# Kernel optimization log

Measured on AMD Instinct MI355X. Metric: run time of the kernel, lower is better.

The kernel has to match this reference:

```python
import jax, jax.numpy as jnp
import numpy as np

N_HEADS = 16
D_MODEL = 1024
TOTAL = 8192
N_SEQ = 8
SEQ_LEN = TOTAL // N_SEQ


def setup_inputs() -> dict:
    key = jax.random.key(0)
    ks = jax.random.split(key, 12)
    f = jnp.float32
    d = D_MODEL
    inp = {
        "query": jax.random.normal(ks[0], (TOTAL, d), f),
        "key": jax.random.normal(ks[1], (TOTAL, d), f),
        "value": jax.random.normal(ks[2], (TOTAL, d), f),
        "seq_lengths_q": jnp.full((N_SEQ,), SEQ_LEN, jnp.int64 if jax.config.jax_enable_x64 else jnp.int32),
        "seq_lengths_kv": jnp.full((N_SEQ,), SEQ_LEN, jnp.int64 if jax.config.jax_enable_x64 else jnp.int32),
        "Wq": jax.random.normal(ks[3], (d, d), f) * 0.02,
        "bq": jnp.zeros((d,), f),
        "Wk": jax.random.normal(ks[4], (d, d), f) * 0.02,
        "bk": jnp.zeros((d,), f),
        "Wv": jax.random.normal(ks[5], (d, d), f) * 0.02,
        "bv": jnp.zeros((d,), f),
        "Wo": jax.random.normal(ks[6], (d, d), f) * 0.02,
        "bo": jnpp if False else jnp.zeros((d,), f),
    }
    return inp


def reference(query, key, value, seq_lengths_q, seq_lengths_kv, Wq, bq, Wk, bk, Wv, bv, Wo, bo):
    Tq, d = query.shape
    Tkv = key.shape[0]
    H = N_HEADS
    Dh = d // H
    B = seq_lengths_q.shape[0]
    Lq = Tq // B  # equal-length packed sequences
    Lkv = Tkv // B
    scale = 1.0 / jnp.sqrt(jnp.asarray(Dh, query.dtype))

    # torch Linear: x @ W.T + b
    Q = (query @ Wq.T + bq).reshape(H, Tq, Dh)   # NOTE: raw view, no transpose
    K = (key @ Wk.T + bk).reshape(H, Tkv, Dh)    # (replicates original's view semantics)
    V = (value @ Wv.T + bv).reshape(H, Tkv, Dh)

    # Block-diagonal mask over equal-length sequences == per-block attention.
    Qb = Q.reshape(H, B, Lq, Dh)
    Kb = K.reshape(H, B, Lkv, Dh)
    Vb = V.reshape(H, B, Lkv, Dh)

    scores = jnp.einsum("hbqd,hbkd->hbqk", Qb, Kb) * scale  # [H,B,Lq,Lkv]
    probs = jax.nn.softmax(scores, axis=-1)
    attn = jnp.einsum("hbqk,hbkd->hbqd", probs, Vb)          # [H,B,Lq,Dh]

    attn = attn.reshape(H, Tq, Dh).reshape(Tq, d)  # matches .view(total_q, d_model)
    out = attn @ Wo.T + bo
    return out
```

## Files before the change

### kernel.cpp

```cpp
#include <hip/hip_runtime.h>
#include <hip/hip_bf16.h>

#define TOTAL   8192
#define DMODEL  1024
#define NHEADS  16
#define NSEQ    8
#define DH      64

typedef float  f32x4 __attribute__((ext_vector_type(4)));
typedef short  s16x8 __attribute__((ext_vector_type(8)));
typedef unsigned short u16;
typedef u16    u16x8 __attribute__((ext_vector_type(8)));
typedef unsigned int u32;
typedef u32    u32x4 __attribute__((ext_vector_type(4)));

__device__ __forceinline__ u16 f2bf_rne(float x) {
  union { float f; unsigned u; } v; v.f = x;
  unsigned r = v.u + 0x7FFFu + ((v.u >> 16) & 1u);
  return (u16)(r >> 16);
}

__device__ __forceinline__ u32 pk_hu(float a, float b) {
  union { float f; u32 u; } A, B; A.f = a; B.f = b;
  return __builtin_amdgcn_perm(B.u + 0x8000u, A.u + 0x8000u, 0x07060302u);
}

__device__ __forceinline__ void async_cp16(const u16* g, u16* l) {
  __builtin_amdgcn_global_load_lds(
      (const __attribute__((address_space(1))) unsigned int*)g,
      (__attribute__((address_space(3))) unsigned int*)l, 16, 0, 0);
}

__device__ __forceinline__ void cvt8_one(const float* __restrict__ src,
                                         u16* __restrict__ dst, long i) {
  float4 a = *reinterpret_cast<const float4*>(src + i);
  float4 b = *reinterpret_cast<const float4*>(src + i + 4);
  u16x8 o;
  o[0] = f2bf_rne(a.x); o[1] = f2bf_rne(a.y); o[2] = f2bf_rne(a.z); o[3] = f2bf_rne(a.w);
  o[4] = f2bf_rne(b.x); o[5] = f2bf_rne(b.y); o[6] = f2bf_rne(b.z); o[7] = f2bf_rne(b.w);
  *reinterpret_cast<u16x8*>(dst + i) = o;
}

__global__ __launch_bounds__(256) void cvt8_w4(const float* __restrict__ w0,
                                               const float* __restrict__ w1,
                                               const float* __restrict__ w2,
                                               const float* __restrict__ w3,
                                               u16* __restrict__ dst) {
  const float* srcs[4] = {w0, w1, w2, w3};
  cvt8_one(srcs[blockIdx.y], dst + (long)blockIdx.y * (DMODEL * (long)DMODEL),
           ((long)blockIdx.x * 256 + threadIdx.x) * 8);
}

__global__ __launch_bounds__(256) void gemm_qkv_f32a(const float* __restrict__ Xq,
                                                     const float* __restrict__ Xk,
                                                     const float* __restrict__ Xv,
                                                     const u16*  __restrict__ W3,
                                                     const float* __restrict__ bq,
                                                     const float* __restrict__ bk,
                                                     const float* __restrict__ bv,
                                                     u16* __restrict__ QKV) {
  __shared__ u16 As[128 * 32];
  __shared__ u16 Bs[128 * 32];
  const int z = blockIdx.z;
  const float* X    = (z == 0) ? Xq : (z == 1) ? Xk : Xv;
  const float* bias = (z == 0) ? bq : (z == 1) ? bk : bv;
  const u16* B = W3 + (long)z * (DMODEL * (long)DMODEL);
  u16* C = QKV + (long)z * (TOTAL * (long)DMODEL);

  const int tid  = threadIdx.x;
  const int lane = tid & 63;
  const int wv   = tid >> 6;
  const int quad = lane >> 4;
  const int m16  = lane & 15;
  const int wm   = (wv & 1) * 64;
  const int wn   = (wv >> 1) * 64;
  const long bm0 = (long)blockIdx.x * 128;
  const long bn0 = (long)blockIdx.y * 128;

  const int arow = tid >> 1;
  const int acol = (tid & 1) * 16;
  const int srow = lane >> 2;
  const int sk8  = (lane & 3) * 8;

  f32x4 acc[4][4] = {};
  const float* Abase = X + (bm0 + arow) * (long)DMODEL + acol;
  const u16*   Bbase = B + bn0 * DMODEL;

  for (int k0 = 0; k0 < DMODEL; k0 += 32) {
    #pragma unroll
    for (int j = 0; j < 2; j++) {
      const int r = j * 4 + wv;
      async_cp16(Bbase + (long)(r * 16 + srow) * DMODEL + k0 + sk8, &Bs[r * 512]);
    }
    {
      const float4* ga = (const float4*)(Abase + k0);
      float4 x0 = ga[0], x1 = ga[1], x2 = ga[2], x3 = ga[3];
      u32x4 p0, p1;
      p0[0] = pk_hu(x0.x, x0.y); p0[1] = pk_hu(x0.z, x0.w);
      p0[2] = pk_hu(x1.x, x1.y); p0[3] = pk_hu(x1.z, x1.w);
      p1[0] = pk_hu(x2.x, x2.y); p1[1] = pk_hu(x2.z, x2.w);
      p1[2] = pk_hu(x3.x, x3.y); p1[3] = pk_hu(x3.z, x3.w);
      *(u32x4*)&As[arow * 32 + acol]     = p0;
      *(u32x4*)&As[arow * 32 + acol + 8] = p1;
    }
    __syncthreads();

    s16x8 af[4], bfr[4];
    #pragma unroll
    for (int i = 0; i < 4; i++)
      af[i] = *(const s16x8*)&As[(wm + i * 16 + m16) * 32 + quad * 8];
    #pragma unroll
    for (int j = 0; j < 4; j++)
      bfr[j] = *(const s16x8*)&Bs[(wn + j * 16 + m16) * 32 + quad * 8];
    #pragma unroll
    for (int i = 0; i < 4; i++)
      #pragma unroll
      for (int j = 0; j < 4; j++)
        acc[i][j] = __builtin_amdgcn_mfma_f32_16x16x32_bf16(af[i], bfr[j], acc[i][j], 0, 0, 0);
    __syncthreads();
  }

  #pragma unroll
  for (int j = 0; j < 4; j++) {
    const long col = bn0 + wn + j * 16 + m16;
    const float bj = bias[col];
    #pragma unroll
    for (int i = 0; i < 4; i++) {
      const long row0 = bm0 + wm + i * 16 + quad * 4;
      #pragma unroll
      for (int r = 0; r < 4; r++)
        C[(row0 + r) * DMODEL + col] = f2bf_rne(acc[i][j][r] + bj);
    }
  }
}

__global__ __launch_bounds__(256) void gemm_out64(const u16* __restrict__ A,
                                                  const u16* __restrict__ B,
                                                  const float* __restrict__ bias,
                                                  float* __restrict__ C) {
  __shared__ u16 As[128 * 64];
  __shared__ u16 Bs[128 * 64];
  const int tid  = threadIdx.x;
  const int lane = tid & 63;
  const int wv   = tid >> 6;
  const int quad = lane >> 4;
  const int m16  = lane & 15;
  const int wm   = (wv & 1) * 64;
  const int wn   = (wv >> 1) * 64;
  const long bm0 = (long)blockIdx.x * 128;
  const long bn0 = (long)blockIdx.y * 128;

  const int r8 = lane >> 3;
  const int c8 = (lane & 7) * 8;

  f32x4 acc[4][4] = {};
  const u16* Abase = A + bm0 * DMODEL;
  const u16* Bbase = B + bn0 * DMODEL;

  for (int k0 = 0; k0 < DMODEL; k0 += 64) {
    #pragma unroll
    for (int j = 0; j < 4; j++) {
      const int rr = j * 4 + wv;
      const long row = rr * 8 + r8;
      async_cp16(Abase + row * DMODEL + k0 + c8, &As[rr * 512]);
      async_cp16(Bbase + row * DMODEL + k0 + c8, &Bs[rr * 512]);
    }
    __syncthreads();

    #pragma unroll
    for (int ks = 0; ks < 2; ks++) {
      s16x8 af[4], bfr[4];
      #pragma unroll
      for (int i = 0; i < 4; i++)
        af[i] = *(const s16x8*)&As[(wm + i * 16 + m16) * 64 + ks * 32 + quad * 8];
      #pragma unroll
      for (int j = 0; j < 4; j++)
        bfr[j] = *(const s16x8*)&Bs[(wn + j * 16 + m16) * 64 + ks * 32 + quad * 8];
      #pragma unroll
      for (int i = 0; i < 4; i++)
        #pragma unroll
        for (int j = 0; j < 4; j++)
          acc[i][j] = __builtin_amdgcn_mfma_f32_16x16x32_bf16(af[i], bfr[j], acc[i][j], 0, 0, 0);
    }
    __syncthreads();
  }

  #pragma unroll
  for (int j = 0; j < 4; j++) {
    const long col = bn0 + wn + j * 16 + m16;
    const float bj = bias[col];
    #pragma unroll
    for (int i = 0; i < 4; i++) {
      const long row0 = bm0 + wm + i * 16 + quad * 4;
      #pragma unroll
      for (int r = 0; r < 4; r++)
        C[(row0 + r) * DMODEL + col] = acc[i][j][r] + bj;
    }
  }
}

__global__ __launch_bounds__(256) void transpose_v(const u16* __restrict__ Vbf,
                                                   u16* __restrict__ Vt) {
  constexpr int TP = 72;
  __shared__ u16 tile[64 * TP];
  const int tid = threadIdx.x;
  const long base = (long)blockIdx.y * 65536;
  const int kt = blockIdx.x;
  {
    int k = tid >> 2, dh0 = (tid & 3) * 16;
    const u16* g = Vbf + base + (long)(kt * 64 + k) * 64 + dh0;
    u16x8 a = ((const u16x8*)g)[0];
    u16x8 b = ((const u16x8*)g)[1];
    #pragma unroll
    for (int i = 0; i < 8; i++) tile[(dh0 + i) * TP + k] = a[i];
    #pragma unroll
    for (int i = 0; i < 8; i++) tile[(dh0 + 8 + i) * TP + k] = b[i];
  }
  __syncthreads();
  {
    int dh = tid >> 2, k0 = (tid & 3) * 16;
    u16x8 a = *(const u16x8*)&tile[dh * TP + k0];
    u16x8 b = *(const u16x8*)&tile[dh * TP + k0 + 8];
    u16* g = Vt + base + (long)dh * 1024 + kt * 64 + k0;
    ((u16x8*)g)[0] = a;
    ((u16x8*)g)[1] = b;
  }
}

__global__ __launch_bounds__(256) void attn_kernel(const u16* __restrict__ Qbf,
                                                   const u16* __restrict__ Kbf,
                                                   const u16* __restrict__ Vt,
                                                   u16* __restrict__ Obf) {
  constexpr int KP = 72;
  __shared__ u16 Ks[64 * KP];
  __shared__ u16 Vs[64 * KP];
  __shared__ u16 Es[4 * 32 * KP];
  const int tid  = threadIdx.x;
  const int lane = tid & 63;
  const int wv   = tid >> 6;
  const int quad = lane >> 4;
  const int m16  = lane & 15;
  const int qt   = blockIdx.y;
  const long base = (long)blockIdx.x * 65536;

  const int qrow0 = qt * 128 + wv * 32;
  s16x8 aq[2][2];
  #pragma unroll
  for (int g = 0; g < 2; g++)
    #pragma unroll
    for (int s = 0; s < 2; s++)
      aq[g][s] = *(const s16x8*)(Qbf + base + (long)(qrow0 + g * 16 + m16) * 64 + s * 32 + quad * 8);

  f32x4 acc_o[2][4] = {};
  f32x4 acc_d[2] = {};

  union { u16x8 u; s16x8 s; } onesu;
  u16 ov = (m16 == 0) ? (u16)0x3F80 : (u16)0;
  #pragma unroll
  for (int i = 0; i < 8; i++) onesu.u[i] = ov;
  const s16x8 bones = onesu.s;

  const float SC = 0.125f * 1.44269504088896340736f;
  const int sr = tid >> 2;
  const int sk = (tid & 3) * 16;

  for (int nt = 0; nt < 16; nt++) {
    {
      const u16* g = Kbf + base + nt * 4096 + (long)sr * 64 + sk;
      u16x8 a = ((const u16x8*)g)[0];
      u16x8 b = ((const u16x8*)g)[1];
      *(u16x8*)&Ks[sr * KP + sk]     = a;
      *(u16x8*)&Ks[sr * KP + sk + 8] = b;
    }
    {
      const u16* g = Vt + base + (long)sr * 1024 + nt * 64 + sk;
      u16x8 a = ((const u16x8*)g)[0];
      u16x8 b = ((const u16x8*)g)[1];
      *(u16x8*)&Vs[sr * KP + sk]     = a;
      *(u16x8*)&Vs[sr * KP + sk + 8] = b;
    }
    __syncthreads();

    #pragma unroll
    for (int n = 0; n < 4; n++) {
      s16x8 bk0 = *(const s16x8*)&Ks[(n * 16 + m16) * KP + quad * 8];
      s16x8 bk1 = *(const s16x8*)&Ks[(n * 16 + m16) * KP + 32 + quad * 8];
      #pragma unroll
      for (int g = 0; g < 2; g++) {
        f32x4 s = {0.f, 0.f, 0.f, 0.f};
        s = __builtin_amdgcn_mfma_f32_16x16x32_bf16(aq[g][0], bk0, s, 0, 0, 0);
        s = __builtin_amdgcn_mfma_f32_16x16x32_bf16(aq[g][1], bk1, s, 0, 0, 0);
        #pragma unroll
        for (int r = 0; r < 4; r++) {
          float e = __builtin_amdgcn_exp2f(s[r] * SC);
          Es[(wv * 32 + g * 16 + quad * 4 + r) * KP + n * 16 + m16] = f2bf_rne(e);
        }
      }
    }
    s16x8 ae[2][2];
    #pragma unroll
    for (int g = 0; g < 2; g++) {
      ae[g][0] = *(const s16x8*)&Es[(wv * 32 + g * 16 + m16) * KP + quad * 8];
      ae[g][1] = *(const s16x8*)&Es[(wv * 32 + g * 16 + m16) * KP + 32 + quad * 8];
    }
    #pragma unroll
    for (int n = 0; n < 4; n++) {
      s16x8 bv0 = *(const s16x8*)&Vs[(n * 16 + m16) * KP + quad * 8];
      s16x8 bv1 = *(const s16x8*)&Vs[(n * 16 + m16) * KP + 32 + quad * 8];
      #pragma unroll
      for (int g = 0; g < 2; g++) {
        acc_o[g][n] = __builtin_amdgcn_mfma_f32_16x16x32_bf16(ae[g][0], bv0, acc_o[g][n], 0, 0, 0);
        acc_o[g][n] = __builtin_amdgcn_mfma_f32_16x16x32_bf16(ae[g][1], bv1, acc_o[g][n], 0, 0, 0);
      }
    }
    #pragma unroll
    for (int g = 0; g < 2; g++) {
      acc_d[g] = __builtin_amdgcn_mfma_f32_16x16x32_bf16(ae[g][0], bones, acc_d[g], 0, 0, 0);
      acc_d[g] = __builtin_amdgcn_mfma_f32_16x16x32_bf16(ae[g][1], bones, acc_d[g], 0, 0, 0);
    }
    __syncthreads();
  }

  #pragma unroll
  for (int g = 0; g < 2; g++)
    #pragma unroll
    for (int r = 0; r < 4; r++) {
      float d = __shfl(acc_d[g][r], lane & 48);
      float rinv = 1.0f / d;
      const long orow = base + (long)(qrow0 + g * 16 + quad * 4 + r) * 64;
      #pragma unroll
      for (int n = 0; n < 4; n++)
        Obf[orow + n * 16 + m16] = f2bf_rne(acc_o[g][n][r] * rinv);
    }
}

extern "C" void kernel_launch(void* const* d_in, const int* in_sizes, int n_in,
                              void* d_out, int out_size, void* d_ws, size_t ws_size,
                              hipStream_t stream) {
  const float* query = (const float*)d_in[0];
  const float* key_  = (const float*)d_in[1];
  const float* value = (const float*)d_in[2];
  const float* Wq = (const float*)d_in[5];
  const float* bq = (const float*)d_in[6];
  const float* Wk = (const float*)d_in[7];
  const float* bk = (const float*)d_in[8];
  const float* Wv = (const float*)d_in[9];
  const float* bv = (const float*)d_in[10];
  const float* Wo = (const float*)d_in[11];
  const float* bo = (const float*)d_in[12];

  char* ws = (char*)d_ws;
  u16* Wbf = (u16*)(ws);
  u16* QKV = (u16*)(ws + (8l << 20));
  u16* Qbf = QKV;
  u16* Kbf = QKV + 1 * (TOTAL * (long)DMODEL);
  u16* Vbf = QKV + 2 * (TOTAL * (long)DMODEL);
  u16* Vt  = (u16*)(ws + (56l << 20));
  u16* Obf = Vbf;

  cvt8_w4<<<dim3(512, 4), 256, 0, stream>>>(Wq, Wk, Wv, Wo, Wbf);
  gemm_qkv_f32a<<<dim3(64, 8, 3), 256, 0, stream>>>(query, key_, value, Wbf,
                                                    bq, bk, bv, QKV);
  transpose_v<<<dim3(16, 128), 256, 0, stream>>>(Vbf, Vt);
  attn_kernel<<<dim3(128, 8), 256, 0, stream>>>(Qbf, Kbf, Vt, Obf);
  gemm_out64<<<dim3(64, 8), 256, 0, stream>>>(Obf, Wbf + 3 * 1048576, bo, (float*)d_out);
}
```

Before: 349.8 us.

## Pre-convert QKV inputs to bf16 and shrink output GEMM tile to 64x128

Adds a separate kernel that converts query/key/value to bf16 before the QKV projection, so the GEMM can load A tiles with async global-to-LDS copies instead of loading fp32 and converting in registers. The output projection GEMM uses 64x128 tiles, doubling the number of blocks. This trades an extra full pass over the activations (read fp32, write bf16) for a simpler, async-loaded GEMM main loop and better occupancy in the output GEMM.

Result: no change. 345.6 us (-1.2%).

```diff
diff --git a/kernel.cpp b/kernel.cpp
--- a/kernel.cpp
+++ b/kernel.cpp
@@ -11,18 +11,11 @@
 typedef short  s16x8 __attribute__((ext_vector_type(8)));
 typedef unsigned short u16;
 typedef u16    u16x8 __attribute__((ext_vector_type(8)));
-typedef unsigned int u32;
-typedef u32    u32x4 __attribute__((ext_vector_type(4)));
 
 __device__ __forceinline__ u16 f2bf_rne(float x) {
   union { float f; unsigned u; } v; v.f = x;
   unsigned r = v.u + 0x7FFFu + ((v.u >> 16) & 1u);
   return (u16)(r >> 16);
-}
-
-__device__ __forceinline__ u32 pk_hu(float a, float b) {
-  union { float f; u32 u; } A, B; A.f = a; B.f = b;
-  return __builtin_amdgcn_perm(B.u + 0x8000u, A.u + 0x8000u, 0x07060302u);
 }
 
 __device__ __forceinline__ void async_cp16(const u16* g, u16* l) {
@@ -51,19 +44,26 @@
            ((long)blockIdx.x * 256 + threadIdx.x) * 8);
 }
 
-__global__ __launch_bounds__(256) void gemm_qkv_f32a(const float* __restrict__ Xq,
-                                                     const float* __restrict__ Xk,
-                                                     const float* __restrict__ Xv,
-                                                     const u16*  __restrict__ W3,
-                                                     const float* __restrict__ bq,
-                                                     const float* __restrict__ bk,
-                                                     const float* __restrict__ bv,
-                                                     u16* __restrict__ QKV) {
+__global__ __launch_bounds__(256) void cvt8_x3(const float* __restrict__ x0,
+                                               const float* __restrict__ x1,
+                                               const float* __restrict__ x2,
+                                               u16* __restrict__ dst) {
+  const float* srcs[3] = {x0, x1, x2};
+  cvt8_one(srcs[blockIdx.y], dst + (long)blockIdx.y * (TOTAL * (long)DMODEL),
+           ((long)blockIdx.x * 256 + threadIdx.x) * 8);
+}
+
+__global__ __launch_bounds__(256) void gemm_qkv(const u16* __restrict__ X3,
+                                                const u16* __restrict__ W3,
+                                                const float* __restrict__ bq,
+                                                const float* __restrict__ bk,
+                                                const float* __restrict__ bv,
+                                                u16* __restrict__ QKV) {
   __shared__ u16 As[128 * 32];
   __shared__ u16 Bs[128 * 32];
   const int z = blockIdx.z;
-  const float* X    = (z == 0) ? Xq : (z == 1) ? Xk : Xv;
   const float* bias = (z == 0) ? bq : (z == 1) ? bk : bv;
+  const u16* A = X3 + (long)z * (TOTAL * (long)DMODEL);
   const u16* B = W3 + (long)z * (DMODEL * (long)DMODEL);
   u16* C = QKV + (long)z * (TOTAL * (long)DMODEL);
 
@@ -77,31 +77,20 @@
   const long bm0 = (long)blockIdx.x * 128;
   const long bn0 = (long)blockIdx.y * 128;
 
-  const int arow = tid >> 1;
-  const int acol = (tid & 1) * 16;
   const int srow = lane >> 2;
   const int sk8  = (lane & 3) * 8;
 
   f32x4 acc[4][4] = {};
-  const float* Abase = X + (bm0 + arow) * (long)DMODEL + acol;
-  const u16*   Bbase = B + bn0 * DMODEL;
+  const u16* Abase = A + bm0 * DMODEL;
+  const u16* Bbase = B + bn0 * DMODEL;
 
   for (int k0 = 0; k0 < DMODEL; k0 += 32) {
     #pragma unroll
     for (int j = 0; j < 2; j++) {
-      const int r = j * 4 + wv;
-      async_cp16(Bbase + (long)(r * 16 + srow) * DMODEL + k0 + sk8, &Bs[r * 512]);
-    }
-    {
-      const float4* ga = (const float4*)(Abase + k0);
-      float4 x0 = ga[0], x1 = ga[1], x2 = ga[2], x3 = ga[3];
-      u32x4 p0, p1;
-      p0[0] = pk_hu(x0.x, x0.y); p0[1] = pk_hu(x0.z, x0.w);
-      p0[2] = pk_hu(x1.x, x1.y); p0[3] = pk_hu(x1.z, x1.w);
-      p1[0] = pk_hu(x2.x, x2.y); p1[1] = pk_hu(x2.z, x2.w);
-      p1[2] = pk_hu(x3.x, x3.y); p1[3] = pk_hu(x3.z, x3.w);
-      *(u32x4*)&As[arow * 32 + acol]     = p0;
-      *(u32x4*)&As[arow * 32 + acol + 8] = p1;
+      const int r   = j * 4 + wv;
+      const int row = r * 16 + srow;
+      async_cp16(Abase + (long)row * DMODEL + k0 + sk8, &As[r * 512]);
+      async_cp16(Bbase + (long)row * DMODEL + k0 + sk8, &Bs[r * 512]);
     }
     __syncthreads();
 
@@ -134,50 +123,53 @@
   }
 }
 
-__global__ __launch_bounds__(256) void gemm_out64(const u16* __restrict__ A,
-                                                  const u16* __restrict__ B,
-                                                  const float* __restrict__ bias,
-                                                  float* __restrict__ C) {
-  __shared__ u16 As[128 * 64];
+__global__ __launch_bounds__(256) void gemm_out_64x128(const u16* __restrict__ A,
+                                                       const u16* __restrict__ B,
+                                                       const float* __restrict__ bias,
+                                                       float* __restrict__ C) {
+  __shared__ u16 As[64 * 64];
   __shared__ u16 Bs[128 * 64];
   const int tid  = threadIdx.x;
   const int lane = tid & 63;
   const int wv   = tid >> 6;
   const int quad = lane >> 4;
   const int m16  = lane & 15;
-  const int wm   = (wv & 1) * 64;
+  const int wm   = (wv & 1) * 32;
   const int wn   = (wv >> 1) * 64;
-  const long bm0 = (long)blockIdx.x * 128;
+  const long bm0 = (long)blockIdx.x * 64;
   const long bn0 = (long)blockIdx.y * 128;
 
   const int r8 = lane >> 3;
   const int c8 = (lane & 7) * 8;
 
-  f32x4 acc[4][4] = {};
+  f32x4 acc[2][4] = {};
   const u16* Abase = A + bm0 * DMODEL;
   const u16* Bbase = B + bn0 * DMODEL;
 
   for (int k0 = 0; k0 < DMODEL; k0 += 64) {
     #pragma unroll
+    for (int j = 0; j < 2; j++) {
+      const int rr = wv * 2 + j;
+      async_cp16(Abase + (long)(rr * 8 + r8) * DMODEL + k0 + c8, &As[rr * 512]);
+    }
+    #pragma unroll
     for (int j = 0; j < 4; j++) {
       const int rr = j * 4 + wv;
-      const long row = rr * 8 + r8;
-      async_cp16(Abase + row * DMODEL + k0 + c8, &As[rr * 512]);
-      async_cp16(Bbase + row * DMODEL + k0 + c8, &Bs[rr * 512]);
+      async_cp16(Bbase + (long)(rr * 8 + r8) * DMODEL + k0 + c8, &Bs[rr * 512]);
     }
     __syncthreads();
 
     #pragma unroll
     for (int ks = 0; ks < 2; ks++) {
-      s16x8 af[4], bfr[4];
-      #pragma unroll
-      for (int i = 0; i < 4; i++)
+      s16x8 af[2], bfr[4];
+      #pragma unroll
+      for (int i = 0; i < 2; i++)
         af[i] = *(const s16x8*)&As[(wm + i * 16 + m16) * 64 + ks * 32 + quad * 8];
       #pragma unroll
       for (int j = 0; j < 4; j++)
         bfr[j] = *(const s16x8*)&Bs[(wn + j * 16 + m16) * 64 + ks * 32 + quad * 8];
       #pragma unroll
-      for (int i = 0; i < 4; i++)
+      for (int i = 0; i < 2; i++)
         #pragma unroll
         for (int j = 0; j < 4; j++)
           acc[i][j] = __builtin_amdgcn_mfma_f32_16x16x32_bf16(af[i], bfr[j], acc[i][j], 0, 0, 0);
@@ -190,7 +182,7 @@
     const long col = bn0 + wn + j * 16 + m16;
     const float bj = bias[col];
     #pragma unroll
-    for (int i = 0; i < 4; i++) {
+    for (int i = 0; i < 2; i++) {
       const long row0 = bm0 + wm + i * 16 + quad * 4;
       #pragma unroll
       for (int r = 0; r < 4; r++)
@@ -355,13 +347,14 @@
   u16* Qbf = QKV;
   u16* Kbf = QKV + 1 * (TOTAL * (long)DMODEL);
   u16* Vbf = QKV + 2 * (TOTAL * (long)DMODEL);
-  u16* Vt  = (u16*)(ws + (56l << 20));
+  u16* X3  = (u16*)(ws + (56l << 20));
+  u16* Vt  = X3;
   u16* Obf = Vbf;
 
   cvt8_w4<<<dim3(512, 4), 256, 0, stream>>>(Wq, Wk, Wv, Wo, Wbf);
-  gemm_qkv_f32a<<<dim3(64, 8, 3), 256, 0, stream>>>(query, key_, value, Wbf,
-                                                    bq, bk, bv, QKV);
+  cvt8_x3<<<dim3(4096, 3), 256, 0, stream>>>(query, key_, value, X3);
+  gemm_qkv<<<dim3(64, 8, 3), 256, 0, stream>>>(X3, Wbf, bq, bk, bv, QKV);
   transpose_v<<<dim3(16, 128), 256, 0, stream>>>(Vbf, Vt);
   attn_kernel<<<dim3(128, 8), 256, 0, stream>>>(Qbf, Kbf, Vt, Obf);
-  gemm_out64<<<dim3(64, 8), 256, 0, stream>>>(Obf, Wbf + 3 * 1048576, bo, (float*)d_out);
-}
+  gemm_out_64x128<<<dim3(128, 8), 256, 0, stream>>>(Obf, Wbf + 3 * 1048576, bo, (float*)d_out);
+}
```
